# Kernel tuning notes

Measured on AMD Instinct MI355X. Metric: run time of the kernel, lower is better.

## Reference

```python
import jax, jax.numpy as jnp
import numpy as np

VOCAB = 1024
EMBED_DIM = 64
COMMIT_COST = 0.25


def setup_inputs() -> dict:
    key = jax.random.key(0)
    k1, k2 = jax.random.split(key)
    z_e = jax.random.normal(k1, (64, 64, 32, 32), dtype=jnp.float32)
    # nn.Embedding init: uniform(-1/vocab, 1/vocab)
    embedding = jax.random.uniform(
        k2, (VOCAB, EMBED_DIM), dtype=jnp.float32,
        minval=-1.0 / VOCAB, maxval=1.0 / VOCAB)
    return {"z_e": z_e, "embedding": embedding}


def reference(z_e, embedding):
    b, d, h, w = z_e.shape
    # [B,D,H,W] -> [N,D]
    flat_z = jnp.transpose(z_e, (0, 2, 3, 1)).reshape(-1, d)
    # squared L2 distances to each code: [N, V]
    distances = (
        jnp.sum(flat_z * flat_z, axis=1, keepdims=True)
        + jnp.sum(embedding * embedding, axis=1)
        - 2.0 * flat_z @ embedding.T
    )
    flat_indices = jnp.argmin(distances, axis=1)
    indices = flat_indices.reshape(b, h, w)
    # gather codes and restore [B,D,H,W]
    z_q = embedding[flat_indices].reshape(b, h, w, d)
    z_q = jnp.transpose(z_q, (0, 3, 1, 2))
    quantization_loss = jnp.mean((z_q - jax.lax.stop_gradient(z_e)) ** 2)
    commitment_loss = jnp.mean((z_e - jax.lax.stop_gradient(z_q)) ** 2) * COMMIT_COST
    z_q_st = z_e + jax.lax.stop_gradient(z_q - z_e)
    # perplexity over codebook usage
    counts = jnp.zeros((VOCAB,), dtype=jnp.float32).at[flat_indices].add(1.0)
    avg_probs = counts / flat_indices.shape[0]
    perplexity = jnp.exp(-jnp.sum(avg_probs * jnp.log(avg_probs + 1e-10)))
    return (z_q_st, indices, quantization_loss, commitment_loss, perplexity)
```

## Files before the change

kernel.cpp:

```cpp
#include <hip/hip_runtime.h>
#include <math.h>

#define VOCAB 1024
#define ED 64
#define NROWS 65536
#define NELEM 4194304
#define MARGIN 2.0e-4f
#define CAPF 8192

typedef __attribute__((ext_vector_type(8))) short short8;
typedef __attribute__((ext_vector_type(4))) float f32x4;

__device__ __forceinline__ unsigned f2bf(float f) {
    unsigned u = __float_as_uint(f);
    u += 0x7fff + ((u >> 16) & 1);
    return u >> 16;
}

__device__ __forceinline__ unsigned long long packkey(float d, int c) {
    unsigned f = __float_as_uint(d);
    unsigned sd = (f & 0x80000000u) ? ~f : (f | 0x80000000u);
    return ((unsigned long long)sd << 32) | (unsigned)c;
}


__global__ void vq_prep(const float* __restrict__ emb, float* __restrict__ e2f,
                        uint4* __restrict__ FB, unsigned* __restrict__ zw1,
                        unsigned* __restrict__ zw2,
                        unsigned long long* __restrict__ kz) {
    const int tid = blockIdx.x * 256 + threadIdx.x;
    for (int i = tid; i < 1028; i += 2048) zw1[i] = 0u;
    for (int i = tid; i < 2304; i += 2048) zw2[i] = 0u;
    for (int i = tid; i < CAPF; i += 2048) kz[i] = ~0ULL;

    if (tid < VOCAB) {
        const float4* src = (const float4*)(emb + tid * ED);
        double s = 0.0;
        #pragma unroll
        for (int g = 0; g < 16; ++g) {
            float4 f = src[g];
            s = fma((double)f.x, (double)f.x, s);
            s = fma((double)f.y, (double)f.y, s);
            s = fma((double)f.z, (double)f.z, s);
            s = fma((double)f.w, (double)f.w, s);
        }
        e2f[tid] = (float)s;
    }
    #pragma unroll
    for (int e = 0; e < 4; ++e) {
        const int i = e * 2048 + tid;
        const int n = i & 15, q = (i >> 4) & 3, kh = (i >> 6) & 1, T = i >> 7;
        const int code = T * 16 + n;
        const int k0 = kh * 32 + q * 8;
        const float4* sp = (const float4*)(emb + code * 64 + k0);
        float4 f0 = sp[0], f1 = sp[1];
        uint4 pk;
        pk.x = f2bf(f0.x) | (f2bf(f0.y) << 16);
        pk.y = f2bf(f0.z) | (f2bf(f0.w) << 16);
        pk.z = f2bf(f1.x) | (f2bf(f1.y) << 16);
        pk.w = f2bf(f1.z) | (f2bf(f1.w) << 16);
        FB[i] = pk;
    }
}

__global__ __launch_bounds__(256, 4)
void vq_filter(const float* __restrict__ z, const float* __restrict__ emb,
               const float* __restrict__ e2f, const uint4* __restrict__ FB,
               float* __restrict__ out, double* __restrict__ lossp,
               unsigned* __restrict__ hist, unsigned* __restrict__ nflag,
               unsigned* __restrict__ rowlist) {
    __shared__ float e2s[1024];
    __shared__ float rowb1[64], rowb2[64];
    __shared__ int   rowi1[64], rowfl[64];
    __shared__ double wls[4];

    const int t = threadIdx.x;
    const int w = t >> 6, lane = t & 63;
    const int q = lane >> 4, n_lo = lane & 15;
    const int bk = blockIdx.x;
    const int n0 = bk * 64;
    const int b  = n0 >> 10;
    const int sb = n0 & 1023;

    #pragma unroll
    for (int i = 0; i < 4; ++i) e2s[i * 256 + t] = e2f[i * 256 + t];

    short8 af[2];
    {
        const int s = sb + w * 16 + n_lo;
        const float* zp = z + (size_t)b * 65536 + s;
        #pragma unroll
        for (int kh = 0; kh < 2; ++kh) {
            short8 fr;
            #pragma unroll
            for (int j = 0; j < 8; ++j) {
                int d = kh * 32 + q * 8 + j;
                fr[j] = (short)f2bf(-2.0f * zp[d * 1024]);
            }
            af[kh] = fr;
        }
    }

    float b1[4], b2[4]; int i1[4];
    #pragma unroll
    for (int sl = 0; sl < 4; ++sl) { b1[sl] = 3.4e38f; b2[sl] = 3.4e38f; i1[sl] = 0; }

    __syncthreads();

    const short8* FBs = (const short8*)FB;
    #pragma unroll 4
    for (int T = 0; T < 64; ++T) {
        short8 bf0 = FBs[T * 128 + lane];
        short8 bf1 = FBs[T * 128 + 64 + lane];
        const int cb = T * 16 + n_lo;
        const float e2 = e2s[cb];
        f32x4 a; a[0] = e2; a[1] = e2; a[2] = e2; a[3] = e2;
        a = __builtin_amdgcn_mfma_f32_16x16x32_bf16(af[0], bf0, a, 0, 0, 0);
        a = __builtin_amdgcn_mfma_f32_16x16x32_bf16(af[1], bf1, a, 0, 0, 0);
        #pragma unroll
        for (int reg = 0; reg < 4; ++reg) {
            float s0 = a[reg];
            b2[reg] = __builtin_amdgcn_fmed3f(s0, b1[reg], b2[reg]);
            bool lt = s0 < b1[reg];
            i1[reg] = lt ? cb : i1[reg];
            b1[reg] = lt ? s0 : b1[reg];
        }
    }

    #pragma unroll
    for (int m = 1; m < 16; m <<= 1) {
        #pragma unroll
        for (int sl = 0; sl < 4; ++sl) {
            float ob1 = __shfl_xor(b1[sl], m, 64);
            int   oi1 = __shfl_xor(i1[sl], m, 64);
            float ob2 = __shfl_xor(b2[sl], m, 64);
            float lose = fmaxf(b1[sl], ob1);
            b2[sl] = fminf(fminf(b2[sl], ob2), lose);
            bool take = (ob1 < b1[sl]) || (ob1 == b1[sl] && oi1 < i1[sl]);
            b1[sl] = take ? ob1 : b1[sl];
            i1[sl] = take ? oi1 : i1[sl];
        }
    }
    if (n_lo == 0) {
        #pragma unroll
        for (int reg = 0; reg < 4; ++reg) {
            int row = w * 16 + q * 4 + reg;
            rowb1[row] = b1[reg];
            rowb2[row] = b2[reg];
            rowi1[row] = i1[reg];
        }
    }
    __syncthreads();

    if (t < 64) {
        const int nrow = n0 + t;
        const int code = rowi1[t];
        const bool want = rowb2[t] < rowb1[t] + MARGIN;
        unsigned long long mask = __ballot(want);
        const int cnt = __popcll(mask);
        unsigned base = 0;
        if (t == 0 && cnt > 0) base = atomicAdd(nflag, (unsigned)cnt);
        base = (unsigned)__shfl((int)base, 0, 64);
        int f = 0;
        if (want) {
            const int rank = __popcll(mask & ((1ULL << t) - 1ULL));
            const unsigned slot = base + (unsigned)rank;
            if (slot < CAPF) { rowlist[slot] = (unsigned)nrow; f = 1; }
        }
        rowfl[t] = f;
        out[NELEM + nrow] = (float)code;
        if (!f) atomicAdd(&hist[code], 1u);
    }
    __syncthreads();

    {
        const int r = lane;
        const int code2 = rowi1[r];
        const bool fl2 = rowfl[r] != 0;
        const int scol = sb + r;
        double lsum = 0.0;
        #pragma unroll
        for (int i = 0; i < 4; ++i) {
            const int d4 = w * 4 + i;
            float4 e4 = *(const float4*)(emb + code2 * 64 + d4 * 4);
            float es[4] = {e4.x, e4.y, e4.z, e4.w};
            #pragma unroll
            for (int j = 0; j < 4; ++j) {
                int d = d4 * 4 + j;
                size_t off = (size_t)b * 65536 + (size_t)d * 1024 + scol;
                float zv = z[off];
                out[off] = zv + (es[j] - zv);
                double df = (double)es[j] - (double)zv;
                lsum = fma(df, df, lsum);
            }
        }
        if (fl2) lsum = 0.0;
        #pragma unroll
        for (int off = 32; off > 0; off >>= 1)
            lsum += __shfl_down(lsum, off, 64);
        if (lane == 0) wls[w] = lsum;
    }
    __syncthreads();
    if (t == 0) lossp[bk] = wls[0] + wls[1] + wls[2] + wls[3];
}

#define EDOT(i) { \
    const f32x4 a4 = *(const f32x4*)(za + (i) * 4); \
    const f32x4 b4 = *(const f32x4*)(zb + (i) * 4); \
    ma = fmaf(a4[0], e##i[0], ma); ma = fmaf(a4[1], e##i[1], ma); \
    ma = fmaf(a4[2], e##i[2], ma); ma = fmaf(a4[3], e##i[3], ma); \
    mb = fmaf(b4[0], e##i[0], mb); mb = fmaf(b4[1], e##i[1], mb); \
    mb = fmaf(b4[2], e##i[2], mb); mb = fmaf(b4[3], e##i[3], mb); }

__global__ __launch_bounds__(256, 2)
void vq_scan(const float* __restrict__ z, const float* __restrict__ emb,
             const float* __restrict__ e2f,
             const unsigned* __restrict__ nflag,
             const unsigned* __restrict__ rowlist,
             unsigned long long* __restrict__ keyws) {
    __shared__ float zs[32 * 64];
    __shared__ float zns[32];
    const int t = threadIdx.x, w = t >> 6, lane = t & 63;
    const int g = (int)(blockIdx.x >> 2), qc = (int)(blockIdx.x & 3);
    unsigned nfr = *nflag;
    const int nf = (int)(nfr < CAPF ? nfr : CAPF);
    if (g * 32 >= nf) return;
    const int nloc = (nf - g * 32 < 32) ? (nf - g * 32) : 32;

    const int c = qc * 256 + w * 64 + lane;
    const f32x4* ep = (const f32x4*)(emb + (size_t)c * 64);
    f32x4 e0 = ep[0],  e1 = ep[1],  e2 = ep[2],  e3 = ep[3];
    f32x4 e4 = ep[4],  e5 = ep[5],  e6 = ep[6],  e7 = ep[7];
    f32x4 e8 = ep[8],  e9 = ep[9],  e10 = ep[10], e11 = ep[11];
    f32x4 e12 = ep[12], e13 = ep[13], e14 = ep[14], e15 = ep[15];
    const float e2c = e2f[c];

    {
        const int r = t >> 3, kb = (t & 7) * 8;
        if (r < nloc) {
            const int row = (int)rowlist[g * 32 + r];
            const int bb = row >> 10, s = row & 1023;
            const float* zp = z + (size_t)bb * 65536 + s;
            #pragma unroll
            for (int k = 0; k < 8; ++k)
                zs[r * 64 + kb + k] = zp[(size_t)(kb + k) * 1024];
        }
    }
    __syncthreads();

    if (t < nloc) {
        double a = 0.0;
        for (int k = 0; k < 64; ++k) {
            double v = (double)zs[t * 64 + k];
            a = fma(v, v, a);
        }
        zns[t] = (float)a;
    }
    __syncthreads();

    for (int r0 = 0; r0 < nloc; r0 += 2) {
        const bool two = (r0 + 1 < nloc);
        const float* za = zs + r0 * 64;
        const float* zb = zs + (two ? r0 + 1 : r0) * 64;
        float ma = 0.f, mb = 0.f;
        EDOT(0)  EDOT(1)  EDOT(2)  EDOT(3)
        EDOT(4)  EDOT(5)  EDOT(6)  EDOT(7)
        EDOT(8)  EDOT(9)  EDOT(10) EDOT(11)
        EDOT(12) EDOT(13) EDOT(14) EDOT(15)

        const float da = (zns[r0] + e2c) - 2.0f * ma;
        unsigned long long ka = packkey(da, c);
        #pragma unroll
        for (int mo = 32; mo > 0; mo >>= 1) {
            unsigned long long o = __shfl_xor(ka, mo, 64);
            if (o < ka) ka = o;
        }
        if (two) {
            const float db = (zns[r0 + 1] + e2c) - 2.0f * mb;
            unsigned long long kb2 = packkey(db, c);
            #pragma unroll
            for (int mo = 32; mo > 0; mo >>= 1) {
                unsigned long long o = __shfl_xor(kb2, mo, 64);
                if (o < kb2) kb2 = o;
            }
            if (lane == 0) atomicMin(&keyws[g * 32 + r0 + 1], kb2);
        }
        if (lane == 0) atomicMin(&keyws[g * 32 + r0], ka);
    }
}

__global__ __launch_bounds__(512, 1)
void vq_fin(const float* __restrict__ z, const float* __restrict__ emb,
            float* __restrict__ out, double* __restrict__ lossp2,
            unsigned* __restrict__ hist,
            const unsigned* __restrict__ nflag,
            const unsigned* __restrict__ rowlist,
            const unsigned long long* __restrict__ keyws) {
    __shared__ int rbi[64];
    __shared__ double lred[8];
    const int t = threadIdx.x, w = t >> 6, lane = t & 63;
    const int g = blockIdx.x;
    unsigned nfr = *nflag;
    const int nf = (int)(nfr < CAPF ? nfr : CAPF);
    if (g * 64 >= nf) return;
    const int nloc = (nf - g * 64 < 64) ? (nf - g * 64) : 64;

    if (t < nloc) {
        const int row = (int)rowlist[g * 64 + t];
        const int code = (int)(unsigned)(keyws[g * 64 + t] & 0xffffffffu);
        rbi[t] = code;
        out[NELEM + row] = (float)code;
        atomicAdd(&hist[code], 1u);
    }
    __syncthreads();

    double lsum = 0.0;
    {
        const int r = t >> 3, d0 = (t & 7) * 8;
        if (r < nloc) {
            const int row = (int)rowlist[g * 64 + r];
            const int bb = row >> 10, s = row & 1023;
            const int code = rbi[r];
            float4 ea = *(const float4*)(emb + code * 64 + d0);
            float4 eb = *(const float4*)(emb + code * 64 + d0 + 4);
            float es[8] = {ea.x, ea.y, ea.z, ea.w, eb.x, eb.y, eb.z, eb.w};
            #pragma unroll
            for (int j = 0; j < 8; ++j) {
                const int d = d0 + j;
                const size_t off = (size_t)bb * 65536 + (size_t)d * 1024 + s;
                const float zv = z[off];
                out[off] = zv + (es[j] - zv);
                double df = (double)es[j] - (double)zv;
                lsum = fma(df, df, lsum);
            }
        }
    }
    #pragma unroll
    for (int o = 32; o > 0; o >>= 1) lsum += __shfl_down(lsum, o, 64);
    if (lane == 0) lred[w] = lsum;
    __syncthreads();
    if (t == 0) {
        double s = 0.0;
        #pragma unroll
        for (int i = 0; i < 8; ++i) s += lred[i];
        lossp2[g] = s;
    }
}

__global__ void vq_finalize_kernel(const unsigned* __restrict__ hist,
                                   const double* __restrict__ lossp,
                                   const double* __restrict__ lossp2,
                                   float* __restrict__ out) {
    __shared__ double red[256], red2[256];
    int t = threadIdx.x;
    double ssum = 0.0, lsum = 0.0;
    for (int i = t; i < VOCAB; i += 256) {
        double p = (double)hist[i] / (double)NROWS;
        ssum += p * log(p + 1e-10);
    }
    for (int i = t; i < 1024; i += 256) lsum += lossp[i];
    if (t < 128) lsum += lossp2[t];
    red[t] = ssum; red2[t] = lsum;
    __syncthreads();
    for (int off = 128; off > 0; off >>= 1) {
        if (t < off) { red[t] += red[t + off]; red2[t] += red2[t + off]; }
        __syncthreads();
    }
    if (t == 0) {
        double qv = red2[0] / (double)NELEM;
        out[NELEM + NROWS + 0] = (float)qv;
        out[NELEM + NROWS + 1] = (float)(qv * 0.25);
        out[NELEM + NROWS + 2] = (float)exp(-red[0]);
    }
}

extern "C" void kernel_launch(void* const* d_in, const int* in_sizes, int n_in,
                              void* d_out, int out_size, void* d_ws, size_t ws_size,
                              hipStream_t stream) {
    const float* z   = (const float*)d_in[0];
    const float* emb = (const float*)d_in[1];
    float* out = (float*)d_out;

    float*              e2f     = (float*)d_ws;
    unsigned*           nfl     = (unsigned*)((char*)d_ws + 4096);
    unsigned*           hist    = (unsigned*)((char*)d_ws + 4112);
    unsigned*           rowlist = (unsigned*)((char*)d_ws + 8208);
    uint4*              FB      = (uint4*)((char*)d_ws + 40976);
    double*             lossp   = (double*)((char*)d_ws + 172048);
    double*             lossp2  = (double*)((char*)d_ws + 180240);
    unsigned long long* keyws   = (unsigned long long*)((char*)d_ws + 181264);
    unsigned*           zw1     = (unsigned*)((char*)d_ws + 4096);
    unsigned*           zw2     = (unsigned*)((char*)d_ws + 172048);

    vq_prep<<<dim3(8), dim3(256), 0, stream>>>(emb, e2f, FB, zw1, zw2, keyws);
    vq_filter<<<dim3(1024), dim3(256), 0, stream>>>(z, emb, e2f, FB, out, lossp,
                                                    hist, nfl, rowlist);
    vq_scan<<<dim3((CAPF / 32) * 4), dim3(256), 0, stream>>>(z, emb, e2f,
                                                             nfl, rowlist, keyws);
    vq_fin<<<dim3(CAPF / 64), dim3(512), 0, stream>>>(z, emb, out, lossp2,
                                                      hist, nfl, rowlist, keyws);
    vq_finalize_kernel<<<dim3(1), dim3(256), 0, stream>>>(hist, lossp, lossp2, out);
}
```

Baseline: 174.6 us.

## Stage codebook in LDS with 128-row filter tiles and fuse rescue scan with finalization

The filter kernel now handles 128 rows per block. Each wave computes two 16-row MFMA tiles that share each codebook fragment, and the bf16 codebook is staged into shared memory in two halves instead of being read from global memory per wave. The separate scan and fin kernels for ambiguous rows are merged into one rescue kernel. It reduces argmin keys in shared memory rather than through global atomicMin, and reuses the staged z values for the output. This removes one launch, the key-buffer initialisation and the redundant codebook and z traffic, at the cost of 64KB+ of LDS, lower occupancy (launch bounds 2), and fewer filter blocks.

Result: no change. 172.5 us (-1.2%).

```diff
diff --git a/kernel.cpp b/kernel.cpp
--- a/kernel.cpp
+++ b/kernel.cpp
@@ -26,12 +26,10 @@
 
 __global__ void vq_prep(const float* __restrict__ emb, float* __restrict__ e2f,
                         uint4* __restrict__ FB, unsigned* __restrict__ zw1,
-                        unsigned* __restrict__ zw2,
-                        unsigned long long* __restrict__ kz) {
+                        unsigned* __restrict__ zw2) {
     const int tid = blockIdx.x * 256 + threadIdx.x;
     for (int i = tid; i < 1028; i += 2048) zw1[i] = 0u;
-    for (int i = tid; i < 2304; i += 2048) zw2[i] = 0u;
-    for (int i = tid; i < CAPF; i += 2048) kz[i] = ~0ULL;
+    for (int i = tid; i < 2560; i += 2048) zw2[i] = 0u;
 
     if (tid < VOCAB) {
         const float4* src = (const float4*)(emb + tid * ED);
@@ -63,31 +61,33 @@
     }
 }
 
-__global__ __launch_bounds__(256, 4)
+__global__ __launch_bounds__(256, 2)
 void vq_filter(const float* __restrict__ z, const float* __restrict__ emb,
                const float* __restrict__ e2f, const uint4* __restrict__ FB,
                float* __restrict__ out, double* __restrict__ lossp,
                unsigned* __restrict__ hist, unsigned* __restrict__ nflag,
                unsigned* __restrict__ rowlist) {
+    __shared__ uint4 Bs4[4096];
     __shared__ float e2s[1024];
-    __shared__ float rowb1[64], rowb2[64];
-    __shared__ int   rowi1[64], rowfl[64];
+    __shared__ float rowb1[128], rowb2[128];
+    __shared__ int   rowi1[128], rowfl[128];
     __shared__ double wls[4];
 
     const int t = threadIdx.x;
     const int w = t >> 6, lane = t & 63;
     const int q = lane >> 4, n_lo = lane & 15;
     const int bk = blockIdx.x;
-    const int n0 = bk * 64;
+    const int n0 = bk * 128;
     const int b  = n0 >> 10;
     const int sb = n0 & 1023;
 
     #pragma unroll
     for (int i = 0; i < 4; ++i) e2s[i * 256 + t] = e2f[i * 256 + t];
 
-    short8 af[2];
-    {
-        const int s = sb + w * 16 + n_lo;
+    short8 af[2][2];
+    #pragma unroll
+    for (int rt = 0; rt < 2; ++rt) {
+        const int s = sb + w * 32 + rt * 16 + n_lo;
         const float* zp = z + (size_t)b * 65536 + s;
         #pragma unroll
         for (int kh = 0; kh < 2; ++kh) {
@@ -97,40 +97,52 @@
                 int d = kh * 32 + q * 8 + j;
                 fr[j] = (short)f2bf(-2.0f * zp[d * 1024]);
             }
-            af[kh] = fr;
-        }
-    }
-
-    float b1[4], b2[4]; int i1[4];
-    #pragma unroll
-    for (int sl = 0; sl < 4; ++sl) { b1[sl] = 3.4e38f; b2[sl] = 3.4e38f; i1[sl] = 0; }
-
-    __syncthreads();
-
-    const short8* FBs = (const short8*)FB;
-    #pragma unroll 4
-    for (int T = 0; T < 64; ++T) {
-        short8 bf0 = FBs[T * 128 + lane];
-        short8 bf1 = FBs[T * 128 + 64 + lane];
-        const int cb = T * 16 + n_lo;
-        const float e2 = e2s[cb];
-        f32x4 a; a[0] = e2; a[1] = e2; a[2] = e2; a[3] = e2;
-        a = __builtin_amdgcn_mfma_f32_16x16x32_bf16(af[0], bf0, a, 0, 0, 0);
-        a = __builtin_amdgcn_mfma_f32_16x16x32_bf16(af[1], bf1, a, 0, 0, 0);
-        #pragma unroll
-        for (int reg = 0; reg < 4; ++reg) {
-            float s0 = a[reg];
-            b2[reg] = __builtin_amdgcn_fmed3f(s0, b1[reg], b2[reg]);
-            bool lt = s0 < b1[reg];
-            i1[reg] = lt ? cb : i1[reg];
-            b1[reg] = lt ? s0 : b1[reg];
+            af[rt][kh] = fr;
+        }
+    }
+
+    float b1[8], b2[8]; int i1[8];
+    #pragma unroll
+    for (int sl = 0; sl < 8; ++sl) { b1[sl] = 3.4e38f; b2[sl] = 3.4e38f; i1[sl] = 0; }
+
+    const short8* FBs = (const short8*)Bs4;
+    for (int h = 0; h < 2; ++h) {
+        __syncthreads();
+        {
+            const uint4* src = FB + h * 4096;
+            #pragma unroll
+            for (int i = 0; i < 16; ++i) Bs4[i * 256 + t] = src[i * 256 + t];
+        }
+        __syncthreads();
+        #pragma unroll 2
+        for (int tt = 0; tt < 32; ++tt) {
+            const int T = h * 32 + tt;
+            short8 bf0 = FBs[tt * 128 + lane];
+            short8 bf1 = FBs[tt * 128 + 64 + lane];
+            const int cb = T * 16 + n_lo;
+            const float e2 = e2s[cb];
+            #pragma unroll
+            for (int rt = 0; rt < 2; ++rt) {
+                f32x4 a; a[0] = e2; a[1] = e2; a[2] = e2; a[3] = e2;
+                a = __builtin_amdgcn_mfma_f32_16x16x32_bf16(af[rt][0], bf0, a, 0, 0, 0);
+                a = __builtin_amdgcn_mfma_f32_16x16x32_bf16(af[rt][1], bf1, a, 0, 0, 0);
+                #pragma unroll
+                for (int reg = 0; reg < 4; ++reg) {
+                    const int sl = rt * 4 + reg;
+                    float s0 = a[reg];
+                    b2[sl] = __builtin_amdgcn_fmed3f(s0, b1[sl], b2[sl]);
+                    bool lt = s0 < b1[sl];
+                    i1[sl] = lt ? cb : i1[sl];
+                    b1[sl] = lt ? s0 : b1[sl];
+                }
+            }
         }
     }
 
     #pragma unroll
     for (int m = 1; m < 16; m <<= 1) {
         #pragma unroll
-        for (int sl = 0; sl < 4; ++sl) {
+        for (int sl = 0; sl < 8; ++sl) {
             float ob1 = __shfl_xor(b1[sl], m, 64);
             int   oi1 = __shfl_xor(i1[sl], m, 64);
             float ob2 = __shfl_xor(b2[sl], m, 64);
@@ -143,27 +155,31 @@
     }
     if (n_lo == 0) {
         #pragma unroll
-        for (int reg = 0; reg < 4; ++reg) {
-            int row = w * 16 + q * 4 + reg;
-            rowb1[row] = b1[reg];
-            rowb2[row] = b2[reg];
-            rowi1[row] = i1[reg];
-        }
-    }
-    __syncthreads();
-
-    if (t < 64) {
+        for (int rt = 0; rt < 2; ++rt) {
+            #pragma unroll
+            for (int reg = 0; reg < 4; ++reg) {
+                int row = w * 32 + rt * 16 + q * 4 + reg;
+                int sl = rt * 4 + reg;
+                rowb1[row] = b1[sl];
+                rowb2[row] = b2[sl];
+                rowi1[row] = i1[sl];
+            }
+        }
+    }
+    __syncthreads();
+
+    if (t < 128) {
         const int nrow = n0 + t;
         const int code = rowi1[t];
         const bool want = rowb2[t] < rowb1[t] + MARGIN;
         unsigned long long mask = __ballot(want);
         const int cnt = __popcll(mask);
         unsigned base = 0;
-        if (t == 0 && cnt > 0) base = atomicAdd(nflag, (unsigned)cnt);
+        if (lane == 0 && cnt > 0) base = atomicAdd(nflag, (unsigned)cnt);
         base = (unsigned)__shfl((int)base, 0, 64);
         int f = 0;
         if (want) {
-            const int rank = __popcll(mask & ((1ULL << t) - 1ULL));
+            const int rank = __popcll(mask & ((1ULL << lane) - 1ULL));
             const unsigned slot = base + (unsigned)rank;
             if (slot < CAPF) { rowlist[slot] = (unsigned)nrow; f = 1; }
         }
@@ -174,14 +190,14 @@
     __syncthreads();
 
     {
-        const int r = lane;
+        const int r = t & 127, tg = t >> 7;
         const int code2 = rowi1[r];
         const bool fl2 = rowfl[r] != 0;
         const int scol = sb + r;
         double lsum = 0.0;
         #pragma unroll
-        for (int i = 0; i < 4; ++i) {
-            const int d4 = w * 4 + i;
+        for (int i = 0; i < 8; ++i) {
+            const int d4 = tg * 8 + i;
             float4 e4 = *(const float4*)(emb + code2 * 64 + d4 * 4);
             float es[4] = {e4.x, e4.y, e4.z, e4.w};
             #pragma unroll
@@ -212,38 +228,34 @@
     mb = fmaf(b4[0], e##i[0], mb); mb = fmaf(b4[1], e##i[1], mb); \
     mb = fmaf(b4[2], e##i[2], mb); mb = fmaf(b4[3], e##i[3], mb); }
 
-__global__ __launch_bounds__(256, 2)
-void vq_scan(const float* __restrict__ z, const float* __restrict__ emb,
-             const float* __restrict__ e2f,
-             const unsigned* __restrict__ nflag,
-             const unsigned* __restrict__ rowlist,
-             unsigned long long* __restrict__ keyws) {
+__global__ __launch_bounds__(512, 1)
+void vq_rescue(const float* __restrict__ z, const float* __restrict__ emb,
+               const float* __restrict__ e2f, float* __restrict__ out,
+               double* __restrict__ lossp2, unsigned* __restrict__ hist,
+               const unsigned* __restrict__ nflag,
+               const unsigned* __restrict__ rowlist) {
     __shared__ float zs[32 * 64];
     __shared__ float zns[32];
+    __shared__ unsigned long long wkey[16][32];
+    __shared__ int rbi[32];
+    __shared__ double lred[8];
+
     const int t = threadIdx.x, w = t >> 6, lane = t & 63;
-    const int g = (int)(blockIdx.x >> 2), qc = (int)(blockIdx.x & 3);
+    const int g = blockIdx.x;
     unsigned nfr = *nflag;
     const int nf = (int)(nfr < CAPF ? nfr : CAPF);
     if (g * 32 >= nf) return;
     const int nloc = (nf - g * 32 < 32) ? (nf - g * 32) : 32;
 
-    const int c = qc * 256 + w * 64 + lane;
-    const f32x4* ep = (const f32x4*)(emb + (size_t)c * 64);
-    f32x4 e0 = ep[0],  e1 = ep[1],  e2 = ep[2],  e3 = ep[3];
-    f32x4 e4 = ep[4],  e5 = ep[5],  e6 = ep[6],  e7 = ep[7];
-    f32x4 e8 = ep[8],  e9 = ep[9],  e10 = ep[10], e11 = ep[11];
-    f32x4 e12 = ep[12], e13 = ep[13], e14 = ep[14], e15 = ep[15];
-    const float e2c = e2f[c];
-
     {
-        const int r = t >> 3, kb = (t & 7) * 8;
+        const int r = t >> 4, k0 = (t & 15) * 4;
         if (r < nloc) {
             const int row = (int)rowlist[g * 32 + r];
             const int bb = row >> 10, s = row & 1023;
             const float* zp = z + (size_t)bb * 65536 + s;
             #pragma unroll
-            for (int k = 0; k < 8; ++k)
-                zs[r * 64 + kb + k] = zp[(size_t)(kb + k) * 1024];
+            for (int k = 0; k < 4; ++k)
+                zs[r * 64 + k0 + k] = zp[(size_t)(k0 + k) * 1024];
         }
     }
     __syncthreads();
@@ -258,67 +270,70 @@
     }
     __syncthreads();
 
-    for (int r0 = 0; r0 < nloc; r0 += 2) {
-        const bool two = (r0 + 1 < nloc);
-        const float* za = zs + r0 * 64;
-        const float* zb = zs + (two ? r0 + 1 : r0) * 64;
-        float ma = 0.f, mb = 0.f;
-        EDOT(0)  EDOT(1)  EDOT(2)  EDOT(3)
-        EDOT(4)  EDOT(5)  EDOT(6)  EDOT(7)
-        EDOT(8)  EDOT(9)  EDOT(10) EDOT(11)
-        EDOT(12) EDOT(13) EDOT(14) EDOT(15)
-
-        const float da = (zns[r0] + e2c) - 2.0f * ma;
-        unsigned long long ka = packkey(da, c);
-        #pragma unroll
-        for (int mo = 32; mo > 0; mo >>= 1) {
-            unsigned long long o = __shfl_xor(ka, mo, 64);
-            if (o < ka) ka = o;
-        }
-        if (two) {
-            const float db = (zns[r0 + 1] + e2c) - 2.0f * mb;
-            unsigned long long kb2 = packkey(db, c);
+    for (int pass = 0; pass < 2; ++pass) {
+        const int c = pass * 512 + w * 64 + lane;
+        const f32x4* ep = (const f32x4*)(emb + (size_t)c * 64);
+        f32x4 e0 = ep[0],  e1 = ep[1],  e2 = ep[2],  e3 = ep[3];
+        f32x4 e4 = ep[4],  e5 = ep[5],  e6 = ep[6],  e7 = ep[7];
+        f32x4 e8 = ep[8],  e9 = ep[9],  e10 = ep[10], e11 = ep[11];
+        f32x4 e12 = ep[12], e13 = ep[13], e14 = ep[14], e15 = ep[15];
+        const float e2c = e2f[c];
+
+        for (int r0 = 0; r0 < nloc; r0 += 2) {
+            const bool two = (r0 + 1 < nloc);
+            const float* za = zs + r0 * 64;
+            const float* zb = zs + (two ? r0 + 1 : r0) * 64;
+            float ma = 0.f, mb = 0.f;
+            EDOT(0)  EDOT(1)  EDOT(2)  EDOT(3)
+            EDOT(4)  EDOT(5)  EDOT(6)  EDOT(7)
+            EDOT(8)  EDOT(9)  EDOT(10) EDOT(11)
+            EDOT(12) EDOT(13) EDOT(14) EDOT(15)
+
+            const float da = (zns[r0] + e2c) - 2.0f * ma;
+            unsigned long long ka = packkey(da, c);
             #pragma unroll
             for (int mo = 32; mo > 0; mo >>= 1) {
-                unsigned long long o = __shfl_xor(kb2, mo, 64);
-                if (o < kb2) kb2 = o;
-            }
-            if (lane == 0) atomicMin(&keyws[g * 32 + r0 + 1], kb2);
-        }
-        if (lane == 0) atomicMin(&keyws[g * 32 + r0], ka);
-    }
-}
-
-__global__ __launch_bounds__(512, 1)
-void vq_fin(const float* __restrict__ z, const float* __restrict__ emb,
-            float* __restrict__ out, double* __restrict__ lossp2,
-            unsigned* __restrict__ hist,
-            const unsigned* __restrict__ nflag,
-            const unsigned* __restrict__ rowlist,
-            const unsigned long long* __restrict__ keyws) {
-    __shared__ int rbi[64];
-    __shared__ double lred[8];
-    const int t = threadIdx.x, w = t >> 6, lane = t & 63;
-    const int g = blockIdx.x;
-    unsigned nfr = *nflag;
-    const int nf = (int)(nfr < CAPF ? nfr : CAPF);
-    if (g * 64 >= nf) return;
-    const int nloc = (nf - g * 64 < 64) ? (nf - g * 64) : 64;
+                unsigned long long o = __shfl_xor(ka, mo, 64);
+                if (o < ka) ka = o;
+            }
+            unsigned long long kb2 = 0;
+            if (two) {
+                const float db = (zns[r0 + 1] + e2c) - 2.0f * mb;
+                kb2 = packkey(db, c);
+                #pragma unroll
+                for (int mo = 32; mo > 0; mo >>= 1) {
+                    unsigned long long o = __shfl_xor(kb2, mo, 64);
+                    if (o < kb2) kb2 = o;
+                }
+            }
+            if (lane == 0) {
+                wkey[pass * 8 + w][r0] = ka;
+                if (two) wkey[pass * 8 + w][r0 + 1] = kb2;
+            }
+        }
+    }
+    __syncthreads();
 
     if (t < nloc) {
-        const int row = (int)rowlist[g * 64 + t];
-        const int code = (int)(unsigned)(keyws[g * 64 + t] & 0xffffffffu);
+        unsigned long long k0 = wkey[0][t];
+        #pragma unroll
+        for (int i = 1; i < 16; ++i) {
+            unsigned long long ki = wkey[i][t];
+            if (ki < k0) k0 = ki;
+        }
+        const int code = (int)(unsigned)(k0 & 0xffffffffu);
         rbi[t] = code;
+        const int row = (int)rowlist[g * 32 + t];
         out[NELEM + row] = (float)code;
         atomicAdd(&hist[code], 1u);
     }
     __syncthreads();
 
     double lsum = 0.0;
-    {
+    if (t < 256) {
         const int r = t >> 3, d0 = (t & 7) * 8;
         if (r < nloc) {
-            const int row = (int)rowlist[g * 64 + r];
+            const int row = (int)rowlist[g * 32 + r];
             const int bb = row >> 10, s = row & 1023;
             const int code = rbi[r];
             float4 ea = *(const float4*)(emb + code * 64 + d0);
@@ -328,7 +343,7 @@
             for (int j = 0; j < 8; ++j) {
                 const int d = d0 + j;
                 const size_t off = (size_t)bb * 65536 + (size_t)d * 1024 + s;
-                const float zv = z[off];
+                const float zv = zs[r * 64 + d];
                 out[off] = zv + (es[j] - zv);
                 double df = (double)es[j] - (double)zv;
                 lsum = fma(df, df, lsum);
@@ -359,7 +374,7 @@
         ssum += p * log(p + 1e-10);
     }
     for (int i = t; i < 1024; i += 256) lsum += lossp[i];
-    if (t < 128) lsum += lossp2[t];
+    lsum += lossp2[t];
     red[t] = ssum; red2[t] = lsum;
     __syncthreads();
     for (int off = 128; off > 0; off >>= 1) {
@@ -381,23 +396,20 @@
     const float* emb = (const float*)d_in[1];
     float* out = (float*)d_out;
 
-    float*              e2f     = (float*)d_ws;
-    unsigned*           nfl     = (unsigned*)((char*)d_ws + 4096);
-    unsigned*           hist    = (unsigned*)((char*)d_ws + 4112);
-    unsigned*           rowlist = (unsigned*)((char*)d_ws + 8208);
-    uint4*              FB      = (uint4*)((char*)d_ws + 40976);
-    double*             lossp   = (double*)((char*)d_ws + 172048);
-    double*             lossp2  = (double*)((char*)d_ws + 180240);
-    unsigned long long* keyws   = (unsigned long long*)((char*)d_ws + 181264);
-    unsigned*           zw1     = (unsigned*)((char*)d_ws + 4096);
-    unsigned*           zw2     = (unsigned*)((char*)d_ws + 172048);
-
-    vq_prep<<<dim3(8), dim3(256), 0, stream>>>(emb, e2f, FB, zw1, zw2, keyws);
-    vq_filter<<<dim3(1024), dim3(256), 0, stream>>>(z, emb, e2f, FB, out, lossp,
-                                                    hist, nfl, rowlist);
-    vq_scan<<<dim3((CAPF / 32) * 4), dim3(256), 0, stream>>>(z, emb, e2f,
-                                                             nfl, rowlist, keyws);
-    vq_fin<<<dim3(CAPF / 64), dim3(512), 0, stream>>>(z, emb, out, lossp2,
-                                                      hist, nfl, rowlist, keyws);
+    float*    e2f     = (float*)d_ws;
+    unsigned* nfl     = (unsigned*)((char*)d_ws + 4096);
+    unsigned* hist    = (unsigned*)((char*)d_ws + 4112);
+    unsigned* rowlist = (unsigned*)((char*)d_ws + 8208);
+    uint4*    FB      = (uint4*)((char*)d_ws + 40976);
+    double*   lossp   = (double*)((char*)d_ws + 172048);
+    double*   lossp2  = (double*)((char*)d_ws + 180240);
+    unsigned* zw1     = (unsigned*)((char*)d_ws + 4096);
+    unsigned* zw2     = (unsigned*)((char*)d_ws + 172048);
+
+    vq_prep<<<dim3(8), dim3(256), 0, stream>>>(emb, e2f, FB, zw1, zw2);
+    vq_filter<<<dim3(512), dim3(256), 0, stream>>>(z, emb, e2f, FB, out, lossp,
+                                                   hist, nfl, rowlist);
+    vq_rescue<<<dim3(256), dim3(512), 0, stream>>>(z, emb, e2f, out, lossp2,
+                                                   hist, nfl, rowlist);
     vq_finalize_kernel<<<dim3(1), dim3(256), 0, stream>>>(hist, lossp, lossp2, out);
 }
```
